# Performance work log

Hardware: AMD Instinct MI355X
Metric: run time of the kernel (lower is better)

## Reference

```python
import jax, jax.numpy as jnp
import numpy as np

B, S, T, DIN, DM, H = 4, 2048, 2048, 256, 512, 8
DH = DM // H
NEG = float(-2**32 + 1)
EPS = 1e-6


def layer_norm(x, g, b):
    mu = jnp.mean(x, axis=-1, keepdims=True)
    var = jnp.mean(jnp.square(x - mu), axis=-1, keepdims=True)
    return (x - mu) * jax.lax.rsqrt(var + EPS) * g + b


def mha(q_in, k_in, v_in, key_mask, wq, bq, wk, bk, wv, bv, w2, b2, g, beta, masked):
    b_, sq, _ = q_in.shape
    sk = k_in.shape[1]
    Q = (q_in @ wq + bq).reshape(b_, sq, H, DH)
    K = (k_in @ wk + bk).reshape(b_, sk, H, DH)
    V = (v_in @ wv + bv).reshape(b_, sk, H, DH)
    scores = jnp.einsum('bqhd,bkhd->bhqk', Q, K) / jnp.sqrt(jnp.float32(DH))
    if masked:
        m = key_mask.astype(jnp.float32).reshape(b_, 1, 1, sk)  # [B,1,1,Tk]
        scores = jnp.where(m == 0, jnp.float32(NEG), scores)
    attn = jax.nn.softmax(scores, axis=-1)  # dropout = identity at inference
    out = jnp.einsum('bhqk,bkhd->bqhd', attn, V).reshape(b_, sq, DM)
    out = out @ w2 + b2 + q_in
    return layer_norm(out, g, beta)


def setup_inputs() -> dict:
    key = jax.random.key(0)
    ks = jax.random.split(key, 16)
    w = lambda k, shp: (jax.random.normal(k, shp, jnp.float32) * 0.02)
    d = {
        'x': jax.random.normal(ks[0], (B, S, DIN), jnp.float32),
        'encoder_output': jax.random.normal(ks[1], (B, T, DIN), jnp.float32),
        'tgt_mask': jax.random.randint(ks[2], (B, S, 1), 0, 2, jnp.int32),
        'src_mask': jax.random.randint(ks[3], (B, T, 1), 0, 2, jnp.int32),
        'm1_wq': w(ks[4], (DIN, DM)), 'm1_bq': jnp.zeros((DM,), jnp.float32),
        'm1_wk': w(ks[5], (DIN, DM)), 'm1_bk': jnp.zeros((DM,), jnp.float32),
        'm1_wv': w(ks[6], (DIN, DM)), 'm1_bv': jnp.zeros((DM,), jnp.float32),
        'm1_w2': w(ks[7], (DM, DIN)), 'm1_b2': jnp.zeros((DIN,), jnp.float32),
        'm1_g': jnp.ones((DIN,), jnp.float32), 'm1_b': jnp.zeros((DIN,), jnp.float32),
        'm2_wq': w(ks[8], (DIN, DM)), 'm2_bq': jnp.zeros((DM,), jnp.float32),
        'm2_wk': w(ks[9], (DIN, DM)), 'm2_bk': jnp.zeros((DM,), jnp.float32),
        'm2_wv': w(ks[10], (DIN, DM)), 'm2_bv': jnp.zeros((DM,), jnp.float32),
        'm2_w2': w(ks[11], (DM, DIN)), 'm2_b2': jnp.zeros((DIN,), jnp.float32),
        'm2_g': jnp.ones((DIN,), jnp.float32), 'm2_b': jnp.zeros((DIN,), jnp.float32),
        'ln1_g': jnp.ones((DIN,), jnp.float32), 'ln1_b': jnp.zeros((DIN,), jnp.float32),
        'ln2_g': jnp.ones((DIN,), jnp.float32), 'ln2_b': jnp.zeros((DIN,), jnp.float32),
        'ln3_g': jnp.ones((DIN,), jnp.float32), 'ln3_b': jnp.zeros((DIN,), jnp.float32),
        'ffn_w1': w(ks[12], (DIN, DM)), 'ffn_b1': jnp.zeros((DM,), jnp.float32),
        'ffn_w2': w(ks[13], (DM, DIN)), 'ffn_b2': jnp.zeros((DIN,), jnp.float32),
    }
    return d


def reference(x, encoder_output, tgt_mask, src_mask,
              m1_wq, m1_bq, m1_wk, m1_bk, m1_wv, m1_bv, m1_w2, m1_b2, m1_g, m1_b,
              m2_wq, m2_bq, m2_wk, m2_bk, m2_wv, m2_bv, m2_w2, m2_b2, m2_g, m2_b,
              ln1_g, ln1_b, ln2_g, ln2_b, ln3_g, ln3_b,
              ffn_w1, ffn_b1, ffn_w2, ffn_b2):
    attn1 = mha(x, x, x, tgt_mask, m1_wq, m1_bq, m1_wk, m1_bk, m1_wv, m1_bv,
                m1_w2, m1_b2, m1_g, m1_b, masked=True)
    x = layer_norm(x + attn1, ln1_g, ln1_b)
    attn2 = mha(x, encoder_output, encoder_output, src_mask,
                m2_wq, m2_bq, m2_wk, m2_bk, m2_wv, m2_bv,
                m2_w2, m2_b2, m2_g, m2_b, masked=False)
    x = layer_norm(x + attn2, ln2_g, ln2_b)
    ffn_out = jax.nn.relu(x @ ffn_w1 + ffn_b1) @ ffn_w2 + ffn_b2
    return layer_norm(x + ffn_out, ln3_g, ln3_b)
```

## Files before the change

### kernel.cpp

```cpp
#include <hip/hip_runtime.h>
#include <hip/hip_bf16.h>

#define B_ 4
#define S_ 2048
#define DIN_ 256
#define DM_ 512
#define H_ 8
#define DH_ 64
#define M_ (B_*S_)

typedef short bf16x8 __attribute__((ext_vector_type(8)));
typedef float f32x4 __attribute__((ext_vector_type(4)));
typedef float f32x16 __attribute__((ext_vector_type(16)));
typedef int v2i __attribute__((ext_vector_type(2)));
typedef unsigned int u32;
typedef unsigned long long u64;

#define MFMA16(a,b,c) __builtin_amdgcn_mfma_f32_16x16x32_bf16((a),(b),(c),0,0,0)
#define MFMA32(a,b,c) __builtin_amdgcn_mfma_f32_32x32x16_bf16((a),(b),(c),0,0,0)

__device__ __forceinline__ unsigned short f2bf(float f) {
  union { float f; unsigned u; } v; v.f = f;
  unsigned r = v.u + 0x7fffu + ((v.u >> 16) & 1u);
  return (unsigned short)(r >> 16);
}
__device__ __forceinline__ f32x4 f32x4_zero() { f32x4 v = {0.f,0.f,0.f,0.f}; return v; }
__device__ __forceinline__ f32x16 f32x16_zero() {
  f32x16 v;
#pragma unroll
  for (int i = 0; i < 16; ++i) v[i] = 0.f;
  return v;
}
__device__ __forceinline__ u32 cvtpk_bf16(float lo, float hi) {
  u32 r; asm("v_cvt_pk_bf16_f32 %0, %1, %2" : "=v"(r) : "v"(lo), "v"(hi)); return r;
}
__device__ __forceinline__ float exp2_asm(float x) {
  float r; asm("v_exp_f32 %0, %1" : "=v"(r) : "v"(x)); return r;
}
__device__ __forceinline__ float max3f(float a, float b, float c) {
  return fmaxf(fmaxf(a, b), c);
}
__device__ __forceinline__ void gload_lds16(const void* g, void* l) {
  __builtin_amdgcn_global_load_lds((const __attribute__((address_space(1))) unsigned int*)g,
                                   (__attribute__((address_space(3))) unsigned int*)l,
                                   16, 0, 0);
}

__global__ void cast_bf16_kernel(const float* __restrict__ in,
                                 unsigned short* __restrict__ out, int n4) {
  int i = blockIdx.x * blockDim.x + threadIdx.x;
  if (i < n4) {
    float4 v = ((const float4*)in)[i];
    ushort4 o;
    o.x = f2bf(v.x); o.y = f2bf(v.y); o.z = f2bf(v.z); o.w = f2bf(v.w);
    ((ushort4*)out)[i] = o;
  }
}

struct WtDesc {
  const float* src[10];
  unsigned short* dst[10];
  int ks[10];
};
__global__ void prep_w_kernel(WtDesc d) {
  int m = blockIdx.y;
  int ks = d.ks[m];
  int K = 1 << ks;
  int N = 131072 >> ks;
  int i = blockIdx.x * 256 + threadIdx.x;
  int n = i >> ks, k = i & (K - 1);
  d.dst[m][i] = f2bf(d.src[m][(size_t)k * N + n]);
}

template<int K, bool RELU>
__global__ __launch_bounds__(256) void gemm_tiled_kernel(
    const unsigned short* __restrict__ A0, const unsigned short* __restrict__ A1,
    const unsigned short* __restrict__ A2,
    const unsigned short* __restrict__ W0, const unsigned short* __restrict__ W1,
    const unsigned short* __restrict__ W2,
    const float* __restrict__ b0, const float* __restrict__ b1, const float* __restrict__ b2,
    unsigned short* __restrict__ o0, unsigned short* __restrict__ o1,
    unsigned short* __restrict__ o2, float scale0, int trsel) {
  const int sel = blockIdx.y >> 2;
  const unsigned short* A = sel == 0 ? A0 : (sel == 1 ? A1 : A2);
  const unsigned short* Wt = sel == 0 ? W0 : (sel == 1 ? W1 : W2);
  const float* bias = sel == 0 ? b0 : (sel == 1 ? b1 : b2);
  unsigned short* out = sel == 0 ? o0 : (sel == 1 ? o1 : o2);
  const float scale = sel == 0 ? scale0 : 1.f;

  const int tid = threadIdx.x;
  const int w = tid >> 6, l = tid & 63;
  const int lr = l & 15, lg = l >> 4;
  const int wr = w >> 1, wc = w & 1;
  const int r0 = blockIdx.x * 128;
  const int c0 = (blockIdx.y & 3) * 128;

  __shared__ __align__(16) unsigned short As[2][128 * 32];
  __shared__ __align__(16) unsigned short Bs[2][128 * 32];

  f32x4 acc[4][4];
#pragma unroll
  for (int m = 0; m < 4; ++m)
#pragma unroll
    for (int n = 0; n < 4; ++n) acc[m][n] = f32x4_zero();

  auto stage = [&](int buf, int k0) {
#pragma unroll
    for (int i = 0; i < 2; ++i) {
      int c = w * 128 + i * 64 + l;
      int row = c >> 2, sl = c & 3;
      gload_lds16(A + (size_t)(r0 + row) * K + k0 + sl * 8,
                  &As[buf][(w * 128 + i * 64) * 8]);
      gload_lds16(Wt + (size_t)(c0 + row) * K + k0 + sl * 8,
                  &Bs[buf][(w * 128 + i * 64) * 8]);
    }
  };

  stage(0, 0);
  __syncthreads();

  const int NT = K / 32;
  for (int t = 0; t < NT; ++t) {
    if (t + 1 < NT) stage((t + 1) & 1, (t + 1) * 32);
    const unsigned short* AB = &As[t & 1][0];
    const unsigned short* BB = &Bs[t & 1][0];
    bf16x8 af[4], bf[4];
#pragma unroll
    for (int m = 0; m < 4; ++m)
      af[m] = *(const bf16x8*)&AB[(wr * 64 + m * 16 + lr) * 32 + lg * 8];
#pragma unroll
    for (int n = 0; n < 4; ++n)
      bf[n] = *(const bf16x8*)&BB[(wc * 64 + n * 16 + lr) * 32 + lg * 8];
#pragma unroll
    for (int m = 0; m < 4; ++m)
#pragma unroll
      for (int n = 0; n < 4; ++n)
        acc[m][n] = MFMA16(af[m], bf[n], acc[m][n]);
    __syncthreads();
  }

  if (sel != trsel) {
#pragma unroll
    for (int n = 0; n < 4; ++n) {
      int col = c0 + wc * 64 + n * 16 + lr;
      float bv = bias[col];
#pragma unroll
      for (int m = 0; m < 4; ++m) {
#pragma unroll
        for (int r = 0; r < 4; ++r) {
          int row = r0 + wr * 64 + m * 16 + lg * 4 + r;
          float v = (acc[m][n][r] + bv) * scale;
          if (RELU) v = fmaxf(v, 0.f);
          out[(size_t)row * DM_ + col] = f2bf(v);
        }
      }
    }
  } else {
    const int bb = r0 / S_;
    const int sbase = r0 - bb * S_ + wr * 64 + lg * 4;
#pragma unroll
    for (int n = 0; n < 4; ++n) {
      int col = c0 + wc * 64 + n * 16 + lr;
      float bv = bias[col];
#pragma unroll
      for (int m = 0; m < 4; ++m) {
        ushort4 o;
#pragma unroll
        for (int r = 0; r < 4; ++r) {
          float v = acc[m][n][r] + bv;
          ((unsigned short*)&o)[r] = f2bf(v);
        }
        *(ushort4*)&out[((size_t)bb * DM_ + col) * S_ + sbase + m * 16] = o;
      }
    }
  }
}

template<int NLN>
__global__ __launch_bounds__(256) void gemm_ln_kernel(
    const unsigned short* __restrict__ A,
    const unsigned short* __restrict__ Wt,
    const float* __restrict__ bias,
    const float* __restrict__ res,
    const float* __restrict__ gA, const float* __restrict__ bA,
    const float* __restrict__ gB, const float* __restrict__ bB,
    float* __restrict__ outF,
    unsigned short* __restrict__ outB) {
  const int tid = threadIdx.x;
  const int w = tid >> 6, l = tid & 63;
  const int lr = l & 15, lg = l >> 4;
  const int r0 = blockIdx.x * 16;

  __shared__ __align__(16) unsigned short Bs[2][256 * 32];
  __shared__ __align__(16) unsigned short As[2][16 * 32];
  __shared__ float ex[16][4][2];

  f32x4 acc[4];
#pragma unroll
  for (int n = 0; n < 4; ++n) acc[n] = f32x4_zero();

  auto stage = [&](int buf, int k0) {
#pragma unroll
    for (int i = 0; i < 4; ++i) {
      int c = w * 256 + i * 64 + l;
      int row = c >> 2, sl = c & 3;
      gload_lds16(Wt + (size_t)row * 512 + k0 + sl * 8,
                  &Bs[buf][(w * 256 + i * 64) * 8]);
    }
    if (w == 0) {
      int row = l >> 2, sl = l & 3;
      gload_lds16(A + (size_t)(r0 + row) * 512 + k0 + sl * 8,
                  &As[buf][0]);
    }
  };

  stage(0, 0);
  __syncthreads();

  for (int t = 0; t < 16; ++t) {
    if (t + 1 < 16) stage((t + 1) & 1, (t + 1) * 32);
    const unsigned short* BB = &Bs[t & 1][0];
    const unsigned short* AB = &As[t & 1][0];
    bf16x8 a = *(const bf16x8*)&AB[lr * 32 + lg * 8];
#pragma unroll
    for (int n = 0; n < 4; ++n) {
      bf16x8 b = *(const bf16x8*)&BB[(w * 64 + n * 16 + lr) * 32 + lg * 8];
      acc[n] = MFMA16(a, b, acc[n]);
    }
    __syncthreads();
  }

  f32x4 rv[4];
#pragma unroll
  for (int n = 0; n < 4; ++n) {
    int col = w * 64 + n * 16 + lr;
    float bv = bias[col];
#pragma unroll
    for (int r = 0; r < 4; ++r) {
      int row = r0 + lg * 4 + r;
      float rr = res[(size_t)row * 256 + col];
      rv[n][r] = rr;
      acc[n][r] += bv + rr;
    }
  }

  auto ln_stats = [&](float* mu, float* rs) {
    float s1[4], s2[4];
#pragma unroll
    for (int r = 0; r < 4; ++r) {
      float a1 = 0.f, a2 = 0.f;
#pragma unroll
      for (int n = 0; n < 4; ++n) { float v = acc[n][r]; a1 += v; a2 += v * v; }
#pragma unroll
      for (int off = 1; off < 16; off <<= 1) {
        a1 += __shfl_xor(a1, off);
        a2 += __shfl_xor(a2, off);
      }
      s1[r] = a1; s2[r] = a2;
    }
    if (lr == 0) {
#pragma unroll
      for (int r = 0; r < 4; ++r) {
        ex[lg * 4 + r][w][0] = s1[r];
        ex[lg * 4 + r][w][1] = s2[r];
      }
    }
    __syncthreads();
#pragma unroll
    for (int r = 0; r < 4; ++r) {
      int row = lg * 4 + r;
      float t1 = ex[row][0][0] + ex[row][1][0] + ex[row][2][0] + ex[row][3][0];
      float t2 = ex[row][0][1] + ex[row][1][1] + ex[row][2][1] + ex[row][3][1];
      float m = t1 * (1.f / 256.f);
      float var = t2 * (1.f / 256.f) - m * m;
      mu[r] = m;
      rs[r] = rsqrtf(var + 1e-6f);
    }
  };

  float mu[4], rs[4];
  ln_stats(mu, rs);

  if constexpr (NLN == 2) {
#pragma unroll
    for (int n = 0; n < 4; ++n) {
      int col = w * 64 + n * 16 + lr;
      float g = gA[col], bb = bA[col];
#pragma unroll
      for (int r = 0; r < 4; ++r) {
        float t1 = (acc[n][r] - mu[r]) * rs[r] * g + bb;
        acc[n][r] = rv[n][r] + t1;
      }
    }
    __syncthreads();
    float mu2[4], rs2[4];
    ln_stats(mu2, rs2);
#pragma unroll
    for (int n = 0; n < 4; ++n) {
      int col = w * 64 + n * 16 + lr;
      float g = gB[col], bb = bB[col];
#pragma unroll
      for (int r = 0; r < 4; ++r) {
        int row = r0 + lg * 4 + r;
        float o = (acc[n][r] - mu2[r]) * rs2[r] * g + bb;
        outF[(size_t)row * 256 + col] = o;
        outB[(size_t)row * 256 + col] = f2bf(o);
      }
    }
  } else {
#pragma unroll
    for (int n = 0; n < 4; ++n) {
      int col = w * 64 + n * 16 + lr;
      float g = gA[col], bb = bA[col];
#pragma unroll
      for (int r = 0; r < 4; ++r) {
        int row = r0 + lg * 4 + r;
        float o = (acc[n][r] - mu[r]) * rs[r] * g + bb;
        outF[(size_t)row * 256 + col] = o;
      }
    }
  }
}

template<bool MASKED>
__global__ __launch_bounds__(256) void flash_kernel(
    const unsigned short* __restrict__ Q,
    const unsigned short* __restrict__ Kg,
    const unsigned short* __restrict__ Vt,
    const int* __restrict__ mask,
    unsigned short* __restrict__ O) {
  __shared__ __align__(16) unsigned short lds[2][2][64 * 64];
  const int tid = threadIdx.x;
  const int w = tid >> 6, l = tid & 63;
  const int q32 = l & 31, hi = l >> 5;
  const int id = blockIdx.x;
  const int g = (id & 7) * 64 + (id >> 3);
  const int bh = g >> 4, xblk = g & 15;
  const int b = bh >> 3, h = bh & 7;
  const size_t bS = (size_t)b * S_;
  const int q0 = xblk * 128 + w * 32;

  bf16x8 qf[4];
  {
    const unsigned short* qp = Q + (bS + q0 + q32) * DM_ + h * DH_;
#pragma unroll
    for (int c = 0; c < 4; ++c) qf[c] = *(const bf16x8*)(qp + c * 16 + hi * 8);
  }
  bf16x8 ones;
#pragma unroll
  for (int j = 0; j < 8; ++j) ones[j] = (short)0x3F80;

  f32x16 o0 = f32x16_zero(), o1 = f32x16_zero();
  float m = -1e30f, lsum = 0.f;

  auto stage = [&](int buf, int kv0) {
#pragma unroll
    for (int p = 0; p < 2; ++p) {
      int i = w * 2 + p;
      int row = i * 8 + (l >> 3);
      int slot = l & 7;
      gload_lds16(Kg + (bS + kv0 + row) * DM_ + h * DH_ + ((slot ^ (row & 7)) * 8),
                  &lds[buf][0][i * 8 * 64]);
      gload_lds16(Vt + ((size_t)b * DM_ + h * DH_ + row) * S_ + kv0 + ((slot ^ (row & 7)) * 8),
                  &lds[buf][1][i * 8 * 64]);
    }
  };

  stage(0, 0);
  int mvCur = 1;
  if (MASKED) mvCur = mask[bS + l];
  __syncthreads();

  const int NT = S_ / 64;
  for (int tt = 0; tt < NT; tt += 2) {
#pragma unroll
    for (int u = 0; u < 2; ++u) {
      const int t = tt + u;
      int mvNext = 1;
      if (t + 1 < NT) {
        stage(u ^ 1, (t + 1) * 64);
        if (MASKED) mvNext = mask[bS + (t + 1) * 64 + l];
      }
      u64 bits = 0;
      if (MASKED) bits = __ballot(mvCur != 0);

      const unsigned short* KB = &lds[u][0][0];
      const unsigned short* VB = &lds[u][1][0];

      f32x16 sc[2];
      __builtin_amdgcn_s_setprio(1);
#pragma unroll
      for (int kt = 0; kt < 2; ++kt) {
        f32x16 s = f32x16_zero();
#pragma unroll
        for (int c = 0; c < 4; ++c) {
          int row = kt * 32 + q32;
          int slot = (c * 2 + hi) ^ (row & 7);
          bf16x8 kf = *(const bf16x8*)&KB[row * 64 + slot * 8];
          s = MFMA32(kf, qf[c], s);
        }
        if (MASKED) {
          u32 valid = (u32)(bits >> (kt * 32 + q32)) & 1u;
          u32 mfw = valid ? 0u : 0xC080C080u;
          union { u32 u[4]; bf16x8 v; } mf;
          mf.u[0] = mfw; mf.u[1] = mfw; mf.u[2] = mfw; mf.u[3] = mfw;
          s = MFMA32(mf.v, ones, s);
        }
        sc[kt] = s;
      }
      __builtin_amdgcn_s_setprio(0);

      float tm;
      {
        float r01;
#pragma unroll
        for (int kt = 0; kt < 2; ++kt) {
          float m0 = max3f(sc[kt][0], sc[kt][1], sc[kt][2]);
          float m1 = max3f(sc[kt][3], sc[kt][4], sc[kt][5]);
          float m2 = max3f(sc[kt][6], sc[kt][7], sc[kt][8]);
          float m3 = max3f(sc[kt][9], sc[kt][10], sc[kt][11]);
          float m4 = max3f(sc[kt][12], sc[kt][13], sc[kt][14]);
          float r = fmaxf(max3f(max3f(m0, m1, m2), m3, m4), sc[kt][15]);
          if (kt == 0) r01 = r; else r01 = fmaxf(r01, r);
        }
        tm = fmaxf(r01, __shfl_xor(r01, 32));
      }

      if (__any(tm > m + 11.5f)) {
        float mn = fmaxf(m, tm);
        float fac = exp2_asm(m - mn);
        m = mn;
        lsum *= fac;
#pragma unroll
        for (int i = 0; i < 16; ++i) {
          int rq = (i & 3) + 8 * (i >> 2) + 4 * hi;
          float fr = __shfl(fac, rq);
          o0[i] *= fr;
          o1[i] *= fr;
        }
      }

      float pv[2][16];
#pragma unroll
      for (int kt = 0; kt < 2; ++kt)
#pragma unroll
        for (int i = 0; i < 16; ++i) pv[kt][i] = exp2_asm(sc[kt][i] - m);

      {
        float s0 = 0.f, s1 = 0.f, s2 = 0.f, s3 = 0.f;
#pragma unroll
        for (int kt = 0; kt < 2; ++kt)
#pragma unroll
          for (int i = 0; i < 16; i += 4) {
            s0 += pv[kt][i]; s1 += pv[kt][i + 1];
            s2 += pv[kt][i + 2]; s3 += pv[kt][i + 3];
          }
        float rsum = (s0 + s1) + (s2 + s3);
        rsum += __shfl_xor(rsum, 32);
        lsum += rsum;
      }

      u32 w8[2][8];
#pragma unroll
      for (int kt = 0; kt < 2; ++kt)
#pragma unroll
        for (int j = 0; j < 8; ++j)
          w8[kt][j] = cvtpk_bf16(pv[kt][2 * j], pv[kt][2 * j + 1]);

      __builtin_amdgcn_s_setprio(1);
#pragma unroll
      for (int kt = 0; kt < 2; ++kt) {
#pragma unroll
        for (int kc = 0; kc < 2; ++kc) {
          v2i r0 = __builtin_amdgcn_permlane32_swap((int)w8[kt][4 * kc + 0],
                                                    (int)w8[kt][4 * kc + 2], false, false);
          v2i r1 = __builtin_amdgcn_permlane32_swap((int)w8[kt][4 * kc + 1],
                                                    (int)w8[kt][4 * kc + 3], false, false);
          union { u32 u[4]; bf16x8 v; } af;
          af.u[0] = (u32)r0.x; af.u[1] = (u32)r1.x; af.u[2] = (u32)r0.y; af.u[3] = (u32)r1.y;
          {
            int row = q32;
            int slot = (kt * 4 + kc * 2 + hi) ^ (row & 7);
            bf16x8 vf = *(const bf16x8*)&VB[row * 64 + slot * 8];
            o0 = MFMA32(af.v, vf, o0);
          }
          {
            int row = 32 + q32;
            int slot = (kt * 4 + kc * 2 + hi) ^ (row & 7);
            bf16x8 vf = *(const bf16x8*)&VB[row * 64 + slot * 8];
            o1 = MFMA32(af.v, vf, o1);
          }
        }
      }
      __builtin_amdgcn_s_setprio(0);
      __syncthreads();
      mvCur = mvNext;
    }
  }

#pragma unroll
  for (int i = 0; i < 16; ++i) {
    int rq = (i & 3) + 8 * (i >> 2) + 4 * hi;
    float ls = __shfl(lsum, rq);
    float inv = __builtin_amdgcn_rcpf(ls);
    int row = q0 + rq;
    O[(bS + row) * DM_ + h * DH_ + q32] = f2bf(o0[i] * inv);
    O[(bS + row) * DM_ + h * DH_ + 32 + q32] = f2bf(o1[i] * inv);
  }
}

extern "C" void kernel_launch(void* const* d_in, const int* in_sizes, int n_in,
                              void* d_out, int out_size, void* d_ws, size_t ws_size,
                              hipStream_t stream) {
  const float* x     = (const float*)d_in[0];
  const float* eo    = (const float*)d_in[1];
  const int*   tmask = (const int*)d_in[2];
  const float* m1_wq = (const float*)d_in[4];  const float* m1_bq = (const float*)d_in[5];
  const float* m1_wk = (const float*)d_in[6];  const float* m1_bk = (const float*)d_in[7];
  const float* m1_wv = (const float*)d_in[8];  const float* m1_bv = (const float*)d_in[9];
  const float* m1_w2 = (const float*)d_in[10]; const float* m1_b2 = (const float*)d_in[11];
  const float* m1_g  = (const float*)d_in[12]; const float* m1_b  = (const float*)d_in[13];
  const float* m2_wq = (const float*)d_in[14]; const float* m2_bq = (const float*)d_in[15];
  const float* m2_wk = (const float*)d_in[16]; const float* m2_bk = (const float*)d_in[17];
  const float* m2_wv = (const float*)d_in[18]; const float* m2_bv = (const float*)d_in[19];
  const float* m2_w2 = (const float*)d_in[20]; const float* m2_b2 = (const float*)d_in[21];
  const float* m2_g  = (const float*)d_in[22]; const float* m2_b  = (const float*)d_in[23];
  const float* ln1_g = (const float*)d_in[24]; const float* ln1_b = (const float*)d_in[25];
  const float* ln2_g = (const float*)d_in[26]; const float* ln2_b = (const float*)d_in[27];
  const float* ln3_g = (const float*)d_in[28]; const float* ln3_b = (const float*)d_in[29];
  const float* f_w1  = (const float*)d_in[30]; const float* f_b1  = (const float*)d_in[31];
  const float* f_w2  = (const float*)d_in[32]; const float* f_b2  = (const float*)d_in[33];

  char* ws = (char*)d_ws;
  size_t off = 0;
  auto alloc = [&](size_t bytes) -> void* {
    void* p = ws + off;
    off += (bytes + 255) & ~(size_t)255;
    return p;
  };
  unsigned short* wt[10];
  for (int i = 0; i < 10; ++i) wt[i] = (unsigned short*)alloc(131072 * 2);
  unsigned short* xb  = (unsigned short*)alloc((size_t)M_ * DIN_ * 2);
  unsigned short* eb  = (unsigned short*)alloc((size_t)M_ * DIN_ * 2);
  unsigned short* Qb  = (unsigned short*)alloc((size_t)M_ * DM_ * 2);
  unsigned short* Kb  = (unsigned short*)alloc((size_t)M_ * DM_ * 2);
  unsigned short* AOb = (unsigned short*)alloc((size_t)M_ * DM_ * 2);
  float*          X1  = (float*)alloc((size_t)M_ * DIN_ * 4);
  unsigned short* X1b = (unsigned short*)alloc((size_t)M_ * DIN_ * 2);
  float*          X2  = (float*)alloc((size_t)M_ * DIN_ * 4);
  unsigned short* X2b = (unsigned short*)alloc((size_t)M_ * DIN_ * 2);
  unsigned short* VtA = (unsigned short*)alloc((size_t)M_ * DM_ * 2);
  unsigned short* VtB = (unsigned short*)alloc((size_t)M_ * DM_ * 2);
  unsigned short* Hb  = Qb;

  int n4 = M_ * DIN_ / 4;
  cast_bf16_kernel<<<n4 / 256, 256, 0, stream>>>(x, xb, n4);
  cast_bf16_kernel<<<n4 / 256, 256, 0, stream>>>(eo, eb, n4);

  WtDesc wd;
  const float* srcs[10] = {m1_wq, m1_wk, m1_wv, m1_w2, m2_wq, m2_wk, m2_wv, m2_w2, f_w1, f_w2};
  int kss[10]           = {8,     8,     8,     9,     8,     8,     8,     9,     8,    9};
  for (int i = 0; i < 10; ++i) { wd.src[i] = srcs[i]; wd.dst[i] = wt[i]; wd.ks[i] = kss[i]; }
  prep_w_kernel<<<dim3(512, 10), 256, 0, stream>>>(wd);

  const int FG = (S_ / 128) * H_ * B_;
  const float QSCALE = 0.125f * 1.44269504088896f;

  gemm_tiled_kernel<256, false><<<dim3(M_ / 128, 12), 256, 0, stream>>>(
      xb, xb, xb, wt[0], wt[1], wt[2], m1_bq, m1_bk, m1_bv, Qb, Kb, VtA, QSCALE, 2);
  flash_kernel<true><<<FG, 256, 0, stream>>>(Qb, Kb, VtA, tmask, AOb);
  gemm_ln_kernel<2><<<M_ / 16, 256, 0, stream>>>(AOb, wt[3], m1_b2, x,
                                                 m1_g, m1_b, ln1_g, ln1_b, X1, X1b);
  gemm_tiled_kernel<256, false><<<dim3(M_ / 128, 12), 256, 0, stream>>>(
      X1b, eb, eb, wt[4], wt[5], wt[6], m2_bq, m2_bk, m2_bv, Qb, Kb, VtB, QSCALE, 2);
  flash_kernel<false><<<FG, 256, 0, stream>>>(Qb, Kb, VtB, nullptr, AOb);
  gemm_ln_kernel<2><<<M_ / 16, 256, 0, stream>>>(AOb, wt[7], m2_b2, X1,
                                                 m2_g, m2_b, ln2_g, ln2_b, X2, X2b);
  gemm_tiled_kernel<256, true><<<dim3(M_ / 128, 4), 256, 0, stream>>>(
      X2b, X2b, X2b, wt[8], wt[8], wt[8], f_b1, f_b1, f_b1, Hb, Hb, Hb, 1.f, -1);
  gemm_ln_kernel<1><<<M_ / 16, 256, 0, stream>>>(Hb, wt[9], f_b2, X2,
                                                 ln3_g, ln3_b, nullptr, nullptr,
                                                 (float*)d_out, nullptr);
}
```

Measured before the change: 207.8 us.

## Widen GEMM-LN K tile with XOR swizzle; compute softmax row sums via MFMA

The GEMM+LayerNorm kernel now stages 64-wide K slices instead of 32, halving the loop iterations and barriers, and XOR-swizzles the LDS layout to avoid bank conflicts. Its LDS footprint roughly doubles, which can lower occupancy. In the attention kernel, the per-row softmax denominator is now accumulated by an extra MFMA of the bf16 probabilities against a ones vector. This replaces the scalar VALU sum and cross-lane shuffle. The cost is one extra MFMA per chunk and summing bf16-rounded probabilities, which keeps numerator and denominator consistent.

Result: faster. 199.6 us (-4.0%).

```diff
diff --git a/kernel.cpp b/kernel.cpp
--- a/kernel.cpp
+++ b/kernel.cpp
@@ -191,8 +191,8 @@
   const int lr = l & 15, lg = l >> 4;
   const int r0 = blockIdx.x * 16;
 
-  __shared__ __align__(16) unsigned short Bs[2][256 * 32];
-  __shared__ __align__(16) unsigned short As[2][16 * 32];
+  __shared__ __align__(16) unsigned short Bs[2][256 * 64];
+  __shared__ __align__(16) unsigned short As[2][16 * 64];
   __shared__ float ex[16][4][2];
 
   f32x4 acc[4];
@@ -201,31 +201,39 @@
 
   auto stage = [&](int buf, int k0) {
 #pragma unroll
-    for (int i = 0; i < 4; ++i) {
-      int c = w * 256 + i * 64 + l;
-      int row = c >> 2, sl = c & 3;
-      gload_lds16(Wt + (size_t)row * 512 + k0 + sl * 8,
-                  &Bs[buf][(w * 256 + i * 64) * 8]);
+    for (int p = 0; p < 8; ++p) {
+      int c = (w * 8 + p) * 64 + l;
+      int row = c >> 3, sl = c & 7;
+      gload_lds16(Wt + (size_t)row * 512 + k0 + ((sl ^ (row & 7)) * 8),
+                  &Bs[buf][(w * 8 + p) * 64 * 8]);
     }
     if (w == 0) {
-      int row = l >> 2, sl = l & 3;
-      gload_lds16(A + (size_t)(r0 + row) * 512 + k0 + sl * 8,
-                  &As[buf][0]);
+#pragma unroll
+      for (int p = 0; p < 2; ++p) {
+        int c = p * 64 + l;
+        int row = c >> 3, sl = c & 7;
+        gload_lds16(A + (size_t)(r0 + row) * 512 + k0 + ((sl ^ (row & 7)) * 8),
+                    &As[buf][p * 64 * 8]);
+      }
     }
   };
 
   stage(0, 0);
   __syncthreads();
 
-  for (int t = 0; t < 16; ++t) {
-    if (t + 1 < 16) stage((t + 1) & 1, (t + 1) * 32);
+  for (int t = 0; t < 8; ++t) {
+    if (t + 1 < 8) stage((t + 1) & 1, (t + 1) * 64);
     const unsigned short* BB = &Bs[t & 1][0];
     const unsigned short* AB = &As[t & 1][0];
-    bf16x8 a = *(const bf16x8*)&AB[lr * 32 + lg * 8];
-#pragma unroll
-    for (int n = 0; n < 4; ++n) {
-      bf16x8 b = *(const bf16x8*)&BB[(w * 64 + n * 16 + lr) * 32 + lg * 8];
-      acc[n] = MFMA16(a, b, acc[n]);
+#pragma unroll
+    for (int kk = 0; kk < 2; ++kk) {
+      bf16x8 a = *(const bf16x8*)&AB[lr * 64 + (((kk * 4 + lg) ^ (lr & 7)) * 8)];
+#pragma unroll
+      for (int n = 0; n < 4; ++n) {
+        int row = w * 64 + n * 16 + lr;
+        bf16x8 b = *(const bf16x8*)&BB[row * 64 + (((kk * 4 + lg) ^ (row & 7)) * 8)];
+        acc[n] = MFMA16(a, b, acc[n]);
+      }
     }
     __syncthreads();
   }
@@ -350,8 +358,8 @@
 #pragma unroll
   for (int j = 0; j < 8; ++j) ones[j] = (short)0x3F80;
 
-  f32x16 o0 = f32x16_zero(), o1 = f32x16_zero();
-  float m = -1e30f, lsum = 0.f;
+  f32x16 o0 = f32x16_zero(), o1 = f32x16_zero(), lacc = f32x16_zero();
+  float m = -1e30f;
 
   auto stage = [&](int buf, int kv0) {
 #pragma unroll
@@ -430,13 +438,13 @@
         float mn = fmaxf(m, tm);
         float fac = exp2_asm(m - mn);
         m = mn;
-        lsum *= fac;
 #pragma unroll
         for (int i = 0; i < 16; ++i) {
           int rq = (i & 3) + 8 * (i >> 2) + 4 * hi;
           float fr = __shfl(fac, rq);
           o0[i] *= fr;
           o1[i] *= fr;
+          lacc[i] *= fr;
         }
       }
 
@@ -445,20 +453,6 @@
       for (int kt = 0; kt < 2; ++kt)
 #pragma unroll
         for (int i = 0; i < 16; ++i) pv[kt][i] = exp2_asm(sc[kt][i] - m);
-
-      {
-        float s0 = 0.f, s1 = 0.f, s2 = 0.f, s3 = 0.f;
-#pragma unroll
-        for (int kt = 0; kt < 2; ++kt)
-#pragma unroll
-          for (int i = 0; i < 16; i += 4) {
-            s0 += pv[kt][i]; s1 += pv[kt][i + 1];
-            s2 += pv[kt][i + 2]; s3 += pv[kt][i + 3];
-          }
-        float rsum = (s0 + s1) + (s2 + s3);
-        rsum += __shfl_xor(rsum, 32);
-        lsum += rsum;
-      }
 
       u32 w8[2][8];
 #pragma unroll
@@ -490,6 +484,7 @@
             bf16x8 vf = *(const bf16x8*)&VB[row * 64 + slot * 8];
             o1 = MFMA32(af.v, vf, o1);
           }
+          lacc = MFMA32(af.v, ones, lacc);
         }
       }
       __builtin_amdgcn_s_setprio(0);
@@ -501,8 +496,7 @@
 #pragma unroll
   for (int i = 0; i < 16; ++i) {
     int rq = (i & 3) + 8 * (i >> 2) + 4 * hi;
-    float ls = __shfl(lsum, rq);
-    float inv = __builtin_amdgcn_rcpf(ls);
+    float inv = __builtin_amdgcn_rcpf(lacc[i]);
     int row = q0 + rq;
     O[(bS + row) * DM_ + h * DH_ + q32] = f2bf(o0[i] * inv);
     O[(bS + row) * DM_ + h * DH_ + 32 + q32] = f2bf(o1[i] * inv);
```
